# Performance work log

Measured on AMD Instinct MI355X. Metric: run time of the kernel, lower is better.

## Reference

```python
import jax, jax.numpy as jnp
import numpy as np

B, S, D = 8, 1024, 512
H = W = 32          # S = H * W, square 2D layout
N, K = 16, 32       # num_heads, head_size


def _reindexed_bias(rel_bias):
    # rel_bias: [N, 2H-1, 2W-1] -> [N, S, S]
    # bias[n, s, t] = rel_bias[n, h_s - h_t + H - 1, w_s - w_t + W - 1]
    pos = jnp.arange(S)
    hh = pos // W
    ww = pos % W
    dh = hh[:, None] - hh[None, :] + (H - 1)  # [S, S] in [0, 2H-2]
    dw = ww[:, None] - ww[None, :] + (W - 1)  # [S, S] in [0, 2W-2]
    return rel_bias[:, dh, dw]  # [N, S, S]


def setup_inputs() -> dict:
    key = jax.random.key(0)
    ks = jax.random.split(key, 10)
    std = 0.02
    query = jax.random.normal(ks[0], (B, S, D), dtype=jnp.float32)
    Wq = jax.random.normal(ks[1], (D, N, K), dtype=jnp.float32) * std
    bq = jnp.zeros((N, K), dtype=jnp.float32)
    Wk = jax.random.normal(ks[2], (D, N, K), dtype=jnp.float32) * std
    bk = jnp.zeros((N, K), dtype=jnp.float32)
    Wv = jax.random.normal(ks[3], (D, N, K), dtype=jnp.float32) * std
    bv = jnp.zeros((N, K), dtype=jnp.float32)
    Wo = jax.random.normal(ks[4], (N, K, D), dtype=jnp.float32) * std
    bo = jnp.zeros((D,), dtype=jnp.float32)
    rel_bias = jax.random.normal(ks[5], (N, 2 * H - 1, 2 * W - 1), dtype=jnp.float32) * std
    return {"query": query, "Wq": Wq, "bq": bq, "Wk": Wk, "bk": bk,
            "Wv": Wv, "bv": bv, "Wo": Wo, "bo": bo, "rel_bias": rel_bias}


def reference(query, Wq, bq, Wk, bk, Wv, bv, Wo, bo, rel_bias):
    q_scale = K ** (-0.5)
    # TrailDense projections: BSD,DNK->BSNK (+ bias)
    q = jnp.einsum('bsd,dnk->bsnk', query, Wq) + bq
    k = jnp.einsum('btd,dnk->btnk', query, Wk) + bk
    v = jnp.einsum('btd,dnk->btnk', query, Wv) + bv
    q = q * q_scale
    logits = jnp.einsum('bsnk,btnk->bnst', q, k)
    logits = logits + _reindexed_bias(rel_bias)[None]  # broadcast over batch
    # float32 softmax, cast back to input dtype
    probs = jax.nn.softmax(logits.astype(jnp.float32), axis=-1).astype(logits.dtype)
    attn_out = jnp.einsum('bnst,btnk->bsnk', probs, v)
    # output projection: BSNK,NKD->BSD (+ bias)
    out = jnp.einsum('bsnk,nkd->bsd', attn_out, Wo) + bo
    return out
```

## Files before the change

### kernel.cpp

```cpp
#include <hip/hip_runtime.h>
#include <stdint.h>


typedef unsigned short u16;
typedef unsigned int   u32;
typedef float  f32x4  __attribute__((ext_vector_type(4)));
typedef float  f32x16 __attribute__((ext_vector_type(16)));
typedef __bf16 bf16x8 __attribute__((ext_vector_type(8)));

#define DEV static __device__ __forceinline__

#if __has_builtin(__builtin_amdgcn_exp2f)
#define EXP2(x) __builtin_amdgcn_exp2f(x)
#else
#define EXP2(x) exp2f(x)
#endif

DEV u16 f2bf(float f){ union { float f; u32 u; } c; c.f = f; u32 x = c.u;
                       return (u16)((x + 0x7fffu + ((x >> 16) & 1u)) >> 16); }
DEV u32 cvtpk(float lo, float hh){
  u32 r; asm("v_cvt_pk_bf16_f32 %0, %1, %2" : "=v"(r) : "v"(lo), "v"(hh));
  return r;
}
DEV void plswap(u32 &a, u32 &b){
  asm("v_permlane32_swap_b32 %0, %1" : "+v"(a), "+v"(b));
}
DEV bf16x8 as_bf8(uint4 v){ return __builtin_bit_cast(bf16x8, v); }

#define LOG2E 1.4426950408889634f

__global__ __launch_bounds__(256) void k_wtrans(
    const float* __restrict__ Wq, const float* __restrict__ Wk,
    const float* __restrict__ Wv, const float* __restrict__ Wo,
    u16* __restrict__ WT)
{
  __shared__ float tile[64][65];
  const float* src = (blockIdx.z == 0) ? Wq : (blockIdx.z == 1) ? Wk
                   : (blockIdx.z == 2) ? Wv : Wo;
  u16* dst = WT + blockIdx.z * 512 * 512;
  const int t = threadIdx.x;
  const int r0 = blockIdx.y * 64, c0 = blockIdx.x * 64;
  #pragma unroll
  for (int p = 0; p < 4; p++){
    int r = p * 16 + (t >> 4), c = (t & 15) * 4;
    float4 v = *(const float4*)&src[(r0 + r) * 512 + c0 + c];
    tile[r][c+0] = v.x; tile[r][c+1] = v.y; tile[r][c+2] = v.z; tile[r][c+3] = v.w;
  }
  __syncthreads();
  #pragma unroll
  for (int p = 0; p < 2; p++){
    int rr = p * 32 + (t >> 3), cc = (t & 7) * 8;
    uint4 v;
    v.x = cvtpk(tile[cc+0][rr], tile[cc+1][rr]);
    v.y = cvtpk(tile[cc+2][rr], tile[cc+3][rr]);
    v.z = cvtpk(tile[cc+4][rr], tile[cc+5][rr]);
    v.w = cvtpk(tile[cc+6][rr], tile[cc+7][rr]);
    *(uint4*)&dst[(c0 + rr) * 512 + r0 + cc] = v;
  }
}

__global__ __launch_bounds__(256) void k_qkv(
    const float* __restrict__ X, const u16* __restrict__ WT,
    const float* __restrict__ bq, const float* __restrict__ bk, const float* __restrict__ bv,
    u16* __restrict__ Qo, u16* __restrict__ Ko, u16* __restrict__ Vt)
{
  __shared__ u16 sm[2][128][72];
  const int mode = blockIdx.z;
  const u16* W = WT + mode * (512 * 512);
  const int m0 = blockIdx.x * 128, n0 = blockIdx.y * 128;
  const int t = threadIdx.x, lane = t & 63, w = t >> 6;
  const int wr = w >> 1, wc = w & 1, lr = lane & 15, hi = lane >> 4;
  f32x4 acc[4][4] = {};
  for (int d0 = 0; d0 < 512; d0 += 64){
    #pragma unroll
    for (int p = 0; p < 8; p++){
      int r = p * 16 + (t >> 4), c4 = (t & 15) * 4;
      float4 v = *(const float4*)&X[(m0 + r) * 512 + d0 + c4];
      uint2 pk2; pk2.x = cvtpk(v.x, v.y); pk2.y = cvtpk(v.z, v.w);
      *(uint2*)&sm[0][r][c4] = pk2;
    }
    #pragma unroll
    for (int p = 0; p < 4; p++){
      int r = p * 32 + (t >> 3), ch = (t & 7) * 8;
      *(uint4*)&sm[1][r][ch] = *(const uint4*)&W[(n0 + r) * 512 + d0 + ch];
    }
    __syncthreads();
    #pragma unroll
    for (int kc = 0; kc < 2; kc++){
      bf16x8 a[4], b[4];
      #pragma unroll
      for (int i = 0; i < 4; i++){
        a[i] = as_bf8(*(const uint4*)&sm[0][wr*64 + i*16 + lr][kc*32 + hi*8]);
        b[i] = as_bf8(*(const uint4*)&sm[1][wc*64 + i*16 + lr][kc*32 + hi*8]);
      }
      #pragma unroll
      for (int i = 0; i < 4; i++)
        #pragma unroll
        for (int j = 0; j < 4; j++)
          acc[i][j] = __builtin_amdgcn_mfma_f32_16x16x32_bf16(a[i], b[j], acc[i][j], 0, 0, 0);
    }
    __syncthreads();
  }
  const float* bias = (mode == 0) ? bq : (mode == 1) ? bk : bv;
  float bv4[4];
  #pragma unroll
  for (int j = 0; j < 4; j++) bv4[j] = bias[n0 + wc*64 + j*16 + lr];

  if (mode < 2){
    u16* Out = (mode == 0) ? Qo : Ko;
    const float scale = (mode == 0) ? (0.17677669529663687f * LOG2E) : 1.0f;
    u16* ep = &sm[0][0][0] + w * 4608;
    #pragma unroll
    for (int i = 0; i < 4; i++)
      #pragma unroll
      for (int j = 0; j < 4; j++)
        #pragma unroll
        for (int r = 0; r < 4; r++){
          float v = (acc[i][j][r] + bv4[j]) * scale;
          ep[(i*16 + hi*4 + r) * 72 + j*16 + lr] = f2bf(v);
        }
    __syncthreads();
    #pragma unroll
    for (int p = 0; p < 8; p++){
      int rr = p * 8 + (lane >> 3), cc = (lane & 7) * 8;
      uint4 v = *(uint4*)&ep[rr * 72 + cc];
      int gm = m0 + wr*64 + rr;
      int gc = n0 + wc*64 + cc;
      int b = gm >> 10, s = gm & 1023, n = gc >> 5, kk = gc & 31;
      *(uint4*)&Out[((b*16 + n)*1024 + s)*32 + kk] = v;
    }
  } else {
    #pragma unroll
    for (int i = 0; i < 4; i++)
      #pragma unroll
      for (int j = 0; j < 4; j++){
        int gm = m0 + wr*64 + i*16 + hi*4;
        int gc = n0 + wc*64 + j*16 + lr;
        int b = gm >> 10, s = gm & 1023, n = gc >> 5, kk = gc & 31;
        uint2 vv;
        vv.x = cvtpk(acc[i][j][0] + bv4[j], acc[i][j][1] + bv4[j]);
        vv.y = cvtpk(acc[i][j][2] + bv4[j], acc[i][j][3] + bv4[j]);
        *(uint2*)&Vt[(((b*16 + n)*32 + kk) * 1024) + s] = vv;
      }
  }
}

__global__ __launch_bounds__(512) void k_attn(
    const u16* __restrict__ Q, const u16* __restrict__ Kg,
    const u16* __restrict__ Vt, const float* __restrict__ relb,
    u16* __restrict__ AO)
{
  __shared__ float bias_s[63 * 63];
  __shared__ float cm[4][16][64];
  __shared__ float lsum_s[4][32];
  const int t = threadIdx.x, lane = t & 63, w8 = t >> 6;
  const int wg = w8 & 3, half = w8 >> 2;
  const int hi = lane >> 5, lq = lane & 31;
  const int bid = ((blockIdx.x & 7) << 7) | (blockIdx.x >> 3);
  const int qt = bid & 7, bn = bid >> 3, n = bn & 15;
  const int q0 = qt * 128 + wg * 32;
  const u16* Qp = Q  + (bn * 1024 + q0) * 32;
  const u16* Kp = Kg + bn * 1024 * 32;
  const u16* Vp = Vt + bn * 32 * 1024;
  const float* rb = relb + n * 63 * 63;
  for (int i = t; i < 63 * 63; i += 512) bias_s[i] = rb[i] * LOG2E - 8.0f;

  bf16x8 qf[2];
  #pragma unroll
  for (int kc = 0; kc < 2; kc++)
    qf[kc] = as_bf8(*(const uint4*)&Qp[lq*32 + kc*16 + hi*8]);
  const int h_q = q0 >> 5;
  __syncthreads();

  f32x16 oacc = {};
  float ls0 = 0.f, ls1 = 0.f;

  const int tbeg = half * 512, tend = tbeg + 512;
  for (int t0 = tbeg; t0 < tend; t0 += 64){
    uint4 kv[4], vv[4];
    #pragma unroll
    for (int ts = 0; ts < 2; ts++){
      kv[ts*2+0] = *(const uint4*)&Kp[(t0 + ts*32 + lq)*32 + hi*8];
      kv[ts*2+1] = *(const uint4*)&Kp[(t0 + ts*32 + lq)*32 + 16 + hi*8];
    }
    #pragma unroll
    for (int tc = 0; tc < 4; tc++)
      vv[tc] = *(const uint4*)&Vp[lq*1024 + t0 + tc*16 + hi*8];

    u32 pk[16];
    #pragma unroll
    for (int ts = 0; ts < 2; ts++){
      f32x16 c = {};
      c = __builtin_amdgcn_mfma_f32_32x32x16_bf16(as_bf8(kv[ts*2+0]), qf[0], c, 0, 0, 0);
      c = __builtin_amdgcn_mfma_f32_32x32x16_bf16(as_bf8(kv[ts*2+1]), qf[1], c, 0, 0, 0);
      const int dh = h_q - (t0 >> 5) - ts + 31;
      const int bbase = dh * 63 + 31 + lq - hi * 4;
      #pragma unroll
      for (int r = 0; r < 16; r += 2){
        int tl = (r & 3) + 8 * (r >> 2);
        float v0 = EXP2(c[r]   + bias_s[bbase - tl]);
        float v1 = EXP2(c[r+1] + bias_s[bbase - tl - 1]);
        ls0 += v0; ls1 += v1;
        pk[ts*8 + (r >> 1)] = cvtpk(v0, v1);
      }
    }
    #pragma unroll
    for (int tc = 0; tc < 4; tc++){
      u32 a0 = pk[tc*4+0], b0 = pk[tc*4+2];
      u32 a1 = pk[tc*4+1], b1 = pk[tc*4+3];
      plswap(a0, b0);
      plswap(a1, b1);
      uint4 bb; bb.x = a0; bb.y = a1; bb.z = b0; bb.w = b1;
      oacc = __builtin_amdgcn_mfma_f32_32x32x16_bf16(as_bf8(vv[tc]), as_bf8(bb), oacc, 0, 0, 0);
    }
  }
  float lsum = ls0 + ls1;
  lsum += __shfl_xor(lsum, 32);

  if (half){
    #pragma unroll
    for (int i = 0; i < 16; i++) cm[wg][i][lane] = oacc[i];
    if (lane < 32) lsum_s[wg][lane] = lsum;
  }
  __syncthreads();
  if (!half){
    #pragma unroll
    for (int i = 0; i < 16; i++) oacc[i] += cm[wg][i][lane];
    lsum += lsum_s[wg][lq];
    float inv = 1.0f / lsum;
    const int b = bn >> 4;
    u16* op = AO + ((b * 1024 + q0 + lq) * 16 + n) * 32;
    #pragma unroll
    for (int g = 0; g < 4; g++){
      uint2 vv2;
      vv2.x = cvtpk(oacc[g*4+0] * inv, oacc[g*4+1] * inv);
      vv2.y = cvtpk(oacc[g*4+2] * inv, oacc[g*4+3] * inv);
      *(uint2*)&op[g*8 + hi*4] = vv2;
    }
  }
}

__global__ __launch_bounds__(256) void k_out(
    const u16* __restrict__ Ain, const u16* __restrict__ WoT,
    const float* __restrict__ bo, float* __restrict__ Out)
{
  __shared__ u16 sm[2][128][72];
  const int m0 = blockIdx.x * 128, n0 = blockIdx.y * 128;
  const int t = threadIdx.x, lane = t & 63, w = t >> 6;
  const int wr = w >> 1, wc = w & 1, lr = lane & 15, hi = lane >> 4;
  f32x4 acc[4][4] = {};
  for (int d0 = 0; d0 < 512; d0 += 64){
    #pragma unroll
    for (int p = 0; p < 4; p++){
      int r = p * 32 + (t >> 3), ch = (t & 7) * 8;
      *(uint4*)&sm[0][r][ch] = *(const uint4*)&Ain[(m0 + r) * 512 + d0 + ch];
      *(uint4*)&sm[1][r][ch] = *(const uint4*)&WoT[(n0 + r) * 512 + d0 + ch];
    }
    __syncthreads();
    #pragma unroll
    for (int kc = 0; kc < 2; kc++){
      bf16x8 a[4], b[4];
      #pragma unroll
      for (int i = 0; i < 4; i++){
        a[i] = as_bf8(*(const uint4*)&sm[0][wr*64 + i*16 + lr][kc*32 + hi*8]);
        b[i] = as_bf8(*(const uint4*)&sm[1][wc*64 + i*16 + lr][kc*32 + hi*8]);
      }
      #pragma unroll
      for (int i = 0; i < 4; i++)
        #pragma unroll
        for (int j = 0; j < 4; j++)
          acc[i][j] = __builtin_amdgcn_mfma_f32_16x16x32_bf16(a[i], b[j], acc[i][j], 0, 0, 0);
    }
    __syncthreads();
  }
  float bv4[4];
  #pragma unroll
  for (int j = 0; j < 4; j++) bv4[j] = bo[n0 + wc*64 + j*16 + lr];
  #pragma unroll
  for (int i = 0; i < 4; i++)
    #pragma unroll
    for (int j = 0; j < 4; j++)
      #pragma unroll
      for (int r = 0; r < 4; r++)
        Out[(m0 + wr*64 + i*16 + hi*4 + r) * 512 + n0 + wc*64 + j*16 + lr]
            = acc[i][j][r] + bv4[j];
}

extern "C" void kernel_launch(void* const* d_in, const int* in_sizes, int n_in,
                              void* d_out, int out_size, void* d_ws, size_t ws_size,
                              hipStream_t stream)
{
  const float* query = (const float*)d_in[0];
  const float* Wq    = (const float*)d_in[1];
  const float* bq    = (const float*)d_in[2];
  const float* Wk    = (const float*)d_in[3];
  const float* bk    = (const float*)d_in[4];
  const float* Wv    = (const float*)d_in[5];
  const float* bv    = (const float*)d_in[6];
  const float* Wo    = (const float*)d_in[7];
  const float* bo    = (const float*)d_in[8];
  const float* relb  = (const float*)d_in[9];
  float* out = (float*)d_out;

  u16* WT  = (u16*)d_ws;
  u16* Qw  = WT  + 4 * 512 * 512;
  u16* Kw  = Qw  + 8 * 16 * 1024 * 32;
  u16* Vtw = Kw  + 8 * 16 * 1024 * 32;
  u16* Aw  = Vtw + 8 * 16 * 1024 * 32;

  k_wtrans<<<dim3(8, 8, 4), dim3(256), 0, stream>>>(Wq, Wk, Wv, Wo, WT);
  k_qkv  <<<dim3(64, 4, 3), dim3(256), 0, stream>>>(query, WT, bq, bk, bv, Qw, Kw, Vtw);
  k_attn <<<dim3(1024),     dim3(512), 0, stream>>>(Qw, Kw, Vtw, relb, Aw);
  k_out  <<<dim3(64, 4),    dim3(256), 0, stream>>>(Aw, WT + 3 * 512 * 512, bo, out);
}
```

Baseline: 94.92 us.

## Load GEMM operands directly from global into registers, dropping LDS staging

```diff
diff --git a/kernel.cpp b/kernel.cpp
--- a/kernel.cpp
+++ b/kernel.cpp
@@ -4,9 +4,9 @@
 
 typedef unsigned short u16;
 typedef unsigned int   u32;
-typedef float  f32x4  __attribute__((ext_vector_type(4)));
-typedef float  f32x16 __attribute__((ext_vector_type(16)));
-typedef __bf16 bf16x8 __attribute__((ext_vector_type(8)));
+typedef float  f32x4   __attribute__((ext_vector_type(4)));
+typedef float  f32x16  __attribute__((ext_vector_type(16)));
+typedef __bf16 bf16x8  __attribute__((ext_vector_type(8)));
 
 #define DEV static __device__ __forceinline__
 
@@ -64,43 +64,44 @@
     const float* __restrict__ bq, const float* __restrict__ bk, const float* __restrict__ bv,
     u16* __restrict__ Qo, u16* __restrict__ Ko, u16* __restrict__ Vt)
 {
-  __shared__ u16 sm[2][128][72];
+  __shared__ u16 ep_s[4][64][72];
   const int mode = blockIdx.z;
   const u16* W = WT + mode * (512 * 512);
   const int m0 = blockIdx.x * 128, n0 = blockIdx.y * 128;
   const int t = threadIdx.x, lane = t & 63, w = t >> 6;
   const int wr = w >> 1, wc = w & 1, lr = lane & 15, hi = lane >> 4;
+
+  const float* xr[4]; const u16* wrow[4];
+  #pragma unroll
+  for (int i = 0; i < 4; i++){
+    xr[i]   = X + (m0 + wr*64 + i*16 + lr) * 512 + hi*8;
+    wrow[i] = W + (n0 + wc*64 + i*16 + lr) * 512 + hi*8;
+  }
+
   f32x4 acc[4][4] = {};
+  #pragma unroll
   for (int d0 = 0; d0 < 512; d0 += 64){
     #pragma unroll
-    for (int p = 0; p < 8; p++){
-      int r = p * 16 + (t >> 4), c4 = (t & 15) * 4;
-      float4 v = *(const float4*)&X[(m0 + r) * 512 + d0 + c4];
-      uint2 pk2; pk2.x = cvtpk(v.x, v.y); pk2.y = cvtpk(v.z, v.w);
-      *(uint2*)&sm[0][r][c4] = pk2;
-    }
-    #pragma unroll
-    for (int p = 0; p < 4; p++){
-      int r = p * 32 + (t >> 3), ch = (t & 7) * 8;
-      *(uint4*)&sm[1][r][ch] = *(const uint4*)&W[(n0 + r) * 512 + d0 + ch];
-    }
-    __syncthreads();
-    #pragma unroll
     for (int kc = 0; kc < 2; kc++){
-      bf16x8 a[4], b[4];
+      bf16x8 a[4]; uint4 b[4];
       #pragma unroll
       for (int i = 0; i < 4; i++){
-        a[i] = as_bf8(*(const uint4*)&sm[0][wr*64 + i*16 + lr][kc*32 + hi*8]);
-        b[i] = as_bf8(*(const uint4*)&sm[1][wc*64 + i*16 + lr][kc*32 + hi*8]);
+        float4 x0 = *(const float4*)(xr[i] + d0 + kc*32);
+        float4 x1 = *(const float4*)(xr[i] + d0 + kc*32 + 4);
+        uint4 av;
+        av.x = cvtpk(x0.x, x0.y); av.y = cvtpk(x0.z, x0.w);
+        av.z = cvtpk(x1.x, x1.y); av.w = cvtpk(x1.z, x1.w);
+        a[i] = as_bf8(av);
+        b[i] = *(const uint4*)(wrow[i] + d0 + kc*32);
       }
       #pragma unroll
       for (int i = 0; i < 4; i++)
         #pragma unroll
         for (int j = 0; j < 4; j++)
-          acc[i][j] = __builtin_amdgcn_mfma_f32_16x16x32_bf16(a[i], b[j], acc[i][j], 0, 0, 0);
-    }
-    __syncthreads();
-  }
+          acc[i][j] = __builtin_amdgcn_mfma_f32_16x16x32_bf16(a[i], as_bf8(b[j]), acc[i][j], 0, 0, 0);
+    }
+  }
+
   const float* bias = (mode == 0) ? bq : (mode == 1) ? bk : bv;
   float bv4[4];
   #pragma unroll
@@ -109,7 +110,7 @@
   if (mode < 2){
     u16* Out = (mode == 0) ? Qo : Ko;
     const float scale = (mode == 0) ? (0.17677669529663687f * LOG2E) : 1.0f;
-    u16* ep = &sm[0][0][0] + w * 4608;
+    u16* ep = &ep_s[w][0][0];
     #pragma unroll
     for (int i = 0; i < 4; i++)
       #pragma unroll
@@ -244,34 +245,34 @@
     const u16* __restrict__ Ain, const u16* __restrict__ WoT,
     const float* __restrict__ bo, float* __restrict__ Out)
 {
-  __shared__ u16 sm[2][128][72];
   const int m0 = blockIdx.x * 128, n0 = blockIdx.y * 128;
   const int t = threadIdx.x, lane = t & 63, w = t >> 6;
   const int wr = w >> 1, wc = w & 1, lr = lane & 15, hi = lane >> 4;
+
+  const u16* ar[4]; const u16* br[4];
+  #pragma unroll
+  for (int i = 0; i < 4; i++){
+    ar[i] = Ain + (m0 + wr*64 + i*16 + lr) * 512 + hi*8;
+    br[i] = WoT + (n0 + wc*64 + i*16 + lr) * 512 + hi*8;
+  }
+
   f32x4 acc[4][4] = {};
+  #pragma unroll
   for (int d0 = 0; d0 < 512; d0 += 64){
     #pragma unroll
-    for (int p = 0; p < 4; p++){
-      int r = p * 32 + (t >> 3), ch = (t & 7) * 8;
-      *(uint4*)&sm[0][r][ch] = *(const uint4*)&Ain[(m0 + r) * 512 + d0 + ch];
-      *(uint4*)&sm[1][r][ch] = *(const uint4*)&WoT[(n0 + r) * 512 + d0 + ch];
-    }
-    __syncthreads();
-    #pragma unroll
     for (int kc = 0; kc < 2; kc++){
-      bf16x8 a[4], b[4];
+      uint4 a[4], b[4];
       #pragma unroll
       for (int i = 0; i < 4; i++){
-        a[i] = as_bf8(*(const uint4*)&sm[0][wr*64 + i*16 + lr][kc*32 + hi*8]);
-        b[i] = as_bf8(*(const uint4*)&sm[1][wc*64 + i*16 + lr][kc*32 + hi*8]);
+        a[i] = *(const uint4*)(ar[i] + d0 + kc*32);
+        b[i] = *(const uint4*)(br[i] + d0 + kc*32);
       }
       #pragma unroll
       for (int i = 0; i < 4; i++)
         #pragma unroll
         for (int j = 0; j < 4; j++)
-          acc[i][j] = __builtin_amdgcn_mfma_f32_16x16x32_bf16(a[i], b[j], acc[i][j], 0, 0, 0);
-    }
-    __syncthreads();
+          acc[i][j] = __builtin_amdgcn_mfma_f32_16x16x32_bf16(as_bf8(a[i]), as_bf8(b[j]), acc[i][j], 0, 0, 0);
+    }
   }
   float bv4[4];
   #pragma unroll
```

New measurement: 169.7 us. 78.8% more time.
